# Kernel tuning notes

Hardware: AMD Instinct MI355X
Metric: run time of the kernel (lower is better)

## Reference

```python
import jax, jax.numpy as jnp
import numpy as np

N_QUBITS = 8
N_LAYERS = 4
N_WIRES = N_QUBITS + 1  # circuit uses an extra ancilla wire
B = 16384
D = 512
LN_EPS = 1e-5


def _rx(theta):
    # RX(t) = [[cos(t/2), -i sin(t/2)], [-i sin(t/2), cos(t/2)]]; theta: () or (B,)
    c = jnp.cos(theta / 2).astype(jnp.complex64)
    s = (-1j) * jnp.sin(theta / 2).astype(jnp.complex64)
    return jnp.stack([jnp.stack([c, s], -1), jnp.stack([s, c], -1)], -2)


def _ry(theta):
    c = jnp.cos(theta / 2).astype(jnp.complex64)
    s = jnp.sin(theta / 2).astype(jnp.complex64)
    return jnp.stack([jnp.stack([c, -s], -1), jnp.stack([s, c], -1)], -2)


def _rz(theta):
    # RZ(t) = diag(e^{-it/2}, e^{it/2})
    half = (theta / 2).astype(jnp.complex64)
    em = jnp.exp(-1j * half)
    ep = jnp.exp(1j * half)
    z = jnp.zeros_like(em)
    return jnp.stack([jnp.stack([em, z], -1), jnp.stack([z, ep], -1)], -2)


def _apply_1q(state, U, wire):
    # state: (B,) + (2,)*N_WIRES ; U: (2,2) shared or (B,2,2) per-sample
    ax = 1 + wire
    s = jnp.moveaxis(state, ax, -1)
    if U.ndim == 2:
        s = jnp.einsum('ij,...j->...i', U, s)
    else:
        s = jnp.einsum('bij,b...j->b...i', U, s)
    return jnp.moveaxis(s, -1, ax)


def _cnot(state, c, t):
    # flip target wire t on the control=1 slice of wire c
    s = jnp.moveaxis(state, (1 + c, 1 + t), (-2, -1))
    s = jnp.stack([s[..., 0, :], jnp.flip(s[..., 1, :], axis=-1)], axis=-2)
    return jnp.moveaxis(s, (-2, -1), (1 + c, 1 + t))


def _quantum_circuit(angles, q_weights):
    # angles: (B, N_QUBITS) per-sample data angles; q_weights: (N_LAYERS, N_QUBITS+1)
    b = angles.shape[0]
    state = jnp.zeros((b, 2 ** N_WIRES), jnp.complex64).at[:, 0].set(1.0)
    state = state.reshape((b,) + (2,) * N_WIRES)
    # data encoding: RX, RZ with per-sample angles
    for i in range(N_QUBITS):
        state = _apply_1q(state, _rx(angles[:, i]), i)
        state = _apply_1q(state, _rz(angles[:, i]), i)
    # first variational layer
    for i in range(N_QUBITS):
        state = _apply_1q(state, _rx(q_weights[0, i]), i)
        state = _apply_1q(state, _rz(q_weights[1, i]), i)
    # entangling layers
    for l in range(1, N_LAYERS):
        for i in range(N_QUBITS):
            state = _cnot(state, i, (i + 1) % N_QUBITS)
            state = _apply_1q(state, _ry(q_weights[l, i]), i)
            state = _apply_1q(state, _rz(q_weights[l, i]), i)
        state = _cnot(state, N_QUBITS - 1, N_QUBITS)
        state = _apply_1q(state, _ry(q_weights[l, -1]), N_QUBITS)
    probs = state.real ** 2 + state.imag ** 2
    # <Z_i> = P(q_i=0) - P(q_i=1)
    zs = []
    for i in range(N_QUBITS):
        axes = tuple(1 + j for j in range(N_WIRES) if j != i)
        p = probs.sum(axes)  # (B, 2)
        zs.append(p[:, 0] - p[:, 1])
    return jnp.stack(zs, axis=1)  # (B, N_QUBITS)


def _forward(x, timestep, w_in, b_in, ln_gamma, ln_beta, q_weights, w_out, b_out):
    h = jnp.tanh(x @ w_in.T + b_in)  # (B, 8)
    mu = h.mean(-1, keepdims=True)
    var = ((h - mu) ** 2).mean(-1, keepdims=True)
    h = (h - mu) / jnp.sqrt(var + LN_EPS) * ln_gamma + ln_beta
    angles = h + timestep  # broadcast scalar timestep
    q_out = _quantum_circuit(angles, q_weights)
    out = q_out @ w_out.T + b_out
    return x + out  # input_dim == output_dim -> residual


def setup_inputs() -> dict:
    key = jax.random.key(0)
    ks = jax.random.split(key, 6)
    x = jax.random.normal(ks[0], (B, D), jnp.float32)
    timestep = jax.random.uniform(ks[1], (1,), jnp.float32)
    w_in = jax.random.normal(ks[2], (N_QUBITS, D), jnp.float32) * np.float32(1.0 / np.sqrt(D))
    b_in = jnp.zeros((N_QUBITS,), jnp.float32)
    ln_gamma = jnp.ones((N_QUBITS,), jnp.float32)
    ln_beta = jnp.zeros((N_QUBITS,), jnp.float32)
    q_weights = jax.random.uniform(ks[3], (N_LAYERS, N_QUBITS + 1), jnp.float32, 0.0, 2.0 * np.pi)
    w_out = jax.random.normal(ks[4], (D, N_QUBITS), jnp.float32) * np.float32(1.0 / np.sqrt(N_QUBITS))
    b_out = jnp.zeros((D,), jnp.float32)
    return {'x': x, 'timestep': timestep, 'w_in': w_in, 'b_in': b_in,
            'ln_gamma': ln_gamma, 'ln_beta': ln_beta, 'q_weights': q_weights,
            'w_out': w_out, 'b_out': b_out}


def reference(x, timestep, w_in, b_in, ln_gamma, ln_beta, q_weights, w_out, b_out):
    return _forward(x, timestep, w_in, b_in, ln_gamma, ln_beta, q_weights, w_out, b_out)
```

## Files before the change

kernel.cpp:

```cpp
#include <hip/hip_runtime.h>
#include <math.h>

#define NSAMP 16384
#define ND    512

typedef float f2 __attribute__((ext_vector_type(2)));
__device__ __forceinline__ f2 spl(float x) { return (f2){x, x}; }

template<int CTRL>
__device__ __forceinline__ float dppf(float x) {
  return __int_as_float(__builtin_amdgcn_update_dpp(
      __float_as_int(x), __float_as_int(x), CTRL, 0xF, 0xF, true));
}
template<int CTRL, int RM, int BM>
__device__ __forceinline__ float dppf_keep(float x) {
  return __int_as_float(__builtin_amdgcn_update_dpp(
      __float_as_int(x), __float_as_int(x), CTRL, RM, BM, false));
}
template<int P>
__device__ __forceinline__ float swzf(float x) {
  return __int_as_float(__builtin_amdgcn_ds_swizzle(__float_as_int(x), P));
}
__device__ __forceinline__ float bpermf(int addrB, float x) {
  return __int_as_float(__builtin_amdgcn_ds_bpermute(addrB, __float_as_int(x)));
}

#if __has_builtin(__builtin_amdgcn_permlane16_swap)
#define HAVE_PLSWAP 1
#endif
__device__ __forceinline__ void plswap16(float x, float& a, float& b) {
#ifdef HAVE_PLSWAP
  auto r = __builtin_amdgcn_permlane16_swap(__float_as_uint(x), __float_as_uint(x), false, false);
  a = __uint_as_float(r[0]); b = __uint_as_float(r[1]);
#else
  a = x; b = swzf<0x401F>(x);
#endif
}
__device__ __forceinline__ void plswap32(float x, float& a, float& b) {
#ifdef HAVE_PLSWAP
  auto r = __builtin_amdgcn_permlane32_swap(__float_as_uint(x), __float_as_uint(x), false, false);
  a = __uint_as_float(r[0]); b = __uint_as_float(r[1]);
#else
  a = x; b = __shfl_xor(x, 32, 64);
#endif
}

template<int M>
__device__ __forceinline__ f2 bfly2(f2 x) {
  f2 r;
  if constexpr (M == 1)       { r.x = dppf<0xB1>(x.x);    r.y = dppf<0xB1>(x.y); }
  else if constexpr (M == 2)  { r.x = dppf<0x4E>(x.x);    r.y = dppf<0x4E>(x.y); }
  else if constexpr (M == 8)  { r.x = dppf<0x128>(x.x);   r.y = dppf<0x128>(x.y); }
  else if constexpr (M == 4)  { r.x = swzf<0x101F>(x.x);  r.y = swzf<0x101F>(x.y); }
  else if constexpr (M == 16) { r.x = swzf<0x401F>(x.x);  r.y = swzf<0x401F>(x.y); }
  else                        { r.x = __shfl_xor(x.x, 32, 64); r.y = __shfl_xor(x.y, 32, 64); }
  return r;
}

__device__ __forceinline__ float fold8_allsum(const float* y, int lane) {
  float v4[4];
#pragma unroll
  for (int i = 0; i < 4; ++i) {
    float keep = (lane & 1) ? y[2 * i + 1] : y[2 * i];
    float send = (lane & 1) ? y[2 * i]     : y[2 * i + 1];
    v4[i] = keep + dppf<0xB1>(send);
  }
  float v2[2];
#pragma unroll
  for (int i = 0; i < 2; ++i) {
    float keep = (lane & 2) ? v4[2 * i + 1] : v4[2 * i];
    float send = (lane & 2) ? v4[2 * i]     : v4[2 * i + 1];
    v2[i] = keep + dppf<0x4E>(send);
  }
  float keep = (lane & 4) ? v2[1] : v2[0];
  float send = (lane & 4) ? v2[0] : v2[1];
  float r = keep + swzf<0x101F>(send);
  r += dppf<0x128>(r);
  { float a, b; plswap16(r, a, b); r = a + b; }
  { float a, b; plswap32(r, a, b); r = a + b; }
  return r;
}

__device__ __forceinline__ float grp8_sum(float x) {
  x += dppf<0xB1>(x);
  x += dppf<0x4E>(x);
  x += swzf<0x101F>(x);
  return x;
}

__device__ __forceinline__ f2 cmul(f2 a, f2 b) {
  f2 bs = __builtin_shufflevector(b, b, 1, 0);
  f2 t  = (f2){-a.y, a.y} * bs;
  return spl(a.x) * b + t;
}

template<int LB>
__device__ __forceinline__ void ry_local(f2* s, float c, float sv) {
#pragma unroll
  for (int r0 = 0; r0 < 8; ++r0) {
    if (r0 & (1 << LB)) continue;
    const int r1 = r0 | (1 << LB);
    f2 a0 = s[r0], a1 = s[r1];
    s[r0] = spl(c) * a0 - spl(sv) * a1;
    s[r1] = spl(sv) * a0 + spl(c) * a1;
  }
}
template<int LB>
__device__ __forceinline__ void rz_local(f2* s, f2 phm, f2 php) {
#pragma unroll
  for (int r = 0; r < 8; ++r) s[r] = cmul(s[r], (r & (1 << LB)) ? php : phm);
}
template<int M>
__device__ __forceinline__ void ry_lane(f2* s, float c, float se) {
#pragma unroll
  for (int r = 0; r < 8; ++r) {
    f2 p = bfly2<M>(s[r]);
    s[r] = spl(c) * s[r] + spl(se) * p;
  }
}
template<int CB, int TB>
__device__ __forceinline__ void cnot_ll(f2* s) {
#pragma unroll
  for (int r0 = 0; r0 < 8; ++r0) {
    if (!(r0 & (1 << CB)) || (r0 & (1 << TB))) continue;
    const int r1 = r0 | (1 << TB);
    f2 t = s[r0]; s[r0] = s[r1]; s[r1] = t;
  }
}
template<int CB, int TM>
__device__ __forceinline__ void cnot_lt(f2* s) {
#pragma unroll
  for (int r = 0; r < 8; ++r) {
    if (!(r & (1 << CB))) continue;
    s[r] = bfly2<TM>(s[r]);
  }
}
__device__ __forceinline__ void cnot_bperm(f2* s, int addrB) {
#pragma unroll
  for (int r = 0; r < 8; ++r) {
    s[r].x = bpermf(addrB, s[r].x);
    s[r].y = bpermf(addrB, s[r].y);
  }
}
__device__ __forceinline__ void cnot_m4_t1(f2* s) {
#pragma unroll
  for (int r = 0; r < 8; ++r) {
    s[r].x = dppf_keep<0xB1, 0xF, 0xA>(s[r].x);
    s[r].y = dppf_keep<0xB1, 0xF, 0xA>(s[r].y);
  }
}
__device__ __forceinline__ void cnot_m1_t2(f2* s) {
#pragma unroll
  for (int r = 0; r < 8; ++r) {
    s[r].x = dppf<0x6C>(s[r].x);
    s[r].y = dppf<0x6C>(s[r].y);
  }
}
template<int TB>
__device__ __forceinline__ void cnot_tl(f2* s, bool cc) {
#pragma unroll
  for (int r0 = 0; r0 < 8; ++r0) {
    if (r0 & (1 << TB)) continue;
    const int r1 = r0 | (1 << TB);
    f2 n0, n1;
    n0.x = cc ? s[r1].x : s[r0].x;  n0.y = cc ? s[r1].y : s[r0].y;
    n1.x = cc ? s[r0].x : s[r1].x;  n1.y = cc ? s[r0].y : s[r1].y;
    s[r0] = n0; s[r1] = n1;
  }
}

__global__ void qpre_kernel(const float* __restrict__ qw, float* __restrict__ ws) {
  int t = threadIdx.x;
  if (t < 27) {
    float s, c; __sincosf(qw[9 + t] * 0.5f, &s, &c);
    ws[2 * t] = c; ws[2 * t + 1] = s;
  }
}

template<bool PRE>
struct Consts {
  const float* qw; const float* ws;
  __device__ __forceinline__ f2 ltrig(int l, int i) const {
    if constexpr (PRE) {
      return ((const f2*)ws)[(l - 1) * 9 + i];
    } else {
      float s, c; __sincosf(qw[l * 9 + i] * 0.5f, &s, &c);
      return (f2){c, s};
    }
  }
};

template<bool PRE, int MODE>
__device__ __forceinline__ void do_layer(f2* st, int lane, const Consts<PRE>& cst, int l,
                                         int addr56, int addr67, int addr78) {
  f2 t[9];
#pragma unroll
  for (int i = 0; i < 9; ++i) t[i] = cst.ltrig(l, i);

  cnot_ll<0, 1>(st);
  ry_local<0>(st, t[0].x, t[0].y);
  rz_local<0>(st, (f2){t[0].x, -t[0].y}, (f2){t[0].x, t[0].y});
  cnot_ll<1, 2>(st);
  ry_local<1>(st, t[1].x, t[1].y);
  cnot_lt<2, 4>(st);
  ry_local<2>(st, t[2].x, t[2].y);
  cnot_m4_t1(st);
  { float se = (lane & 4) ? t[3].y : -t[3].y;
    ry_lane<4>(st, t[3].x, se); }
  cnot_m1_t2(st);
  { float se = (lane & 1) ? t[4].y : -t[4].y;
    ry_lane<1>(st, t[4].x, se); }
  cnot_bperm(st, addr56);
  { float se = (lane & 2) ? t[5].y : -t[5].y;
    ry_lane<2>(st, t[5].x, se); }
  cnot_bperm(st, addr67);
  { float se = (lane & 8) ? t[6].y : -t[6].y;
    ry_lane<8>(st, t[6].x, se); }
  cnot_tl<0>(st, (lane & 16) != 0);
  { float se = (lane & 16) ? t[7].y : -t[7].y;
    ry_lane<16>(st, t[7].x, se); }

  if constexpr (MODE == 1) {
    const float wsel = (lane & 32) ? ((lane & 16) ? t[8].x : t[8].y)
                                   : ((lane & 16) ? -t[8].y : t[8].x);
#pragma unroll
    for (int r = 0; r < 8; ++r) st[r] = st[r] * spl(wsel);
  }
  if constexpr (MODE == 2) {
    cnot_bperm(st, addr78);
  }
  if constexpr (MODE != 3) {
    f2 L4[4];
#pragma unroll
    for (int k = 0; k < 4; ++k) {
      f2 p1 = (f2){t[1].x, (k & 1) ? t[1].y : -t[1].y};
      f2 p2 = (f2){t[2].x, (k & 2) ? t[2].y : -t[2].y};
      L4[k] = cmul(p1, p2);
    }
    f2 phW = (f2){t[3].x, (lane & 4)  ? t[3].y : -t[3].y};
    phW = cmul(phW, (f2){t[4].x, (lane & 1)  ? t[4].y : -t[4].y});
    phW = cmul(phW, (f2){t[5].x, (lane & 2)  ? t[5].y : -t[5].y});
    phW = cmul(phW, (f2){t[6].x, (lane & 8)  ? t[6].y : -t[6].y});
    phW = cmul(phW, (f2){t[7].x, (lane & 16) ? t[7].y : -t[7].y});
    f2 pr[4];
#pragma unroll
    for (int k = 0; k < 4; ++k) pr[k] = cmul(L4[k], phW);
#pragma unroll
    for (int r = 0; r < 8; ++r) st[r] = cmul(st[r], pr[(r >> 1) & 3]);
  }
}

template<bool PRE>
__global__ __launch_bounds__(256, 4) void qlayer_kernel(
    const float* __restrict__ x, const float* __restrict__ tstep,
    const float* __restrict__ w_in, const float* __restrict__ b_in,
    const float* __restrict__ g, const float* __restrict__ be,
    const float* __restrict__ qw, const float* __restrict__ w_out,
    const float* __restrict__ b_out, float* __restrict__ out,
    const float* __restrict__ ws)
{
  __shared__ __align__(16) float s_u[4][8][4];
  __shared__ __align__(16) float s_z[4][8];

  const int tid    = threadIdx.x;
  const int lane   = tid & 63;
  const int wv     = tid >> 6;
  const int sample = blockIdx.x * 4 + wv;
  const int jq     = lane & 7;
  const int dbase  = lane << 3;

  const int addr56 = (lane ^ ((lane & 2) << 2)) << 2;
  const int addr67 = (lane ^ ((lane & 8) << 1)) << 2;
  const int addr78 = (lane ^ ((lane & 16) << 1)) << 2;

  const float4* xr4 = (const float4*)(x + (size_t)sample * ND + dbase);
  const float4 xa = xr4[0], xb = xr4[1];
  const f2 xp0 = (f2){xa.x, xa.y}, xp1 = (f2){xa.z, xa.w};
  const f2 xp2 = (f2){xb.x, xb.y}, xp3 = (f2){xb.z, xb.w};

  float h[8];
#pragma unroll
  for (int j = 0; j < 8; ++j) {
    const float4* wj = (const float4*)(w_in + j * ND + dbase);
    float4 wa = wj[0], wb = wj[1];
    f2 acc = xp0 * (f2){wa.x, wa.y};
    acc += xp1 * (f2){wa.z, wa.w};
    acc += xp2 * (f2){wb.x, wb.y};
    acc += xp3 * (f2){wb.z, wb.w};
    h[j] = acc.x + acc.y;
  }
  const float H = fold8_allsum(h, lane);

  const float t0 = tstep[0];
  float tj;
  {
    float v = H + b_in[jq];
    v = fminf(15.f, fmaxf(-15.f, v));
    float e2 = __expf(2.f * v);
    tj = (e2 - 1.f) * __builtin_amdgcn_rcpf(e2 + 1.f);
  }
  const float mu = grp8_sum(tj) * 0.125f;
  const float dv = tj - mu;
  const float var = grp8_sum(dv * dv) * 0.125f;
  const float rstd = rsqrtf(var + 1e-5f);
  const float ang = dv * rstd * g[jq] + be[jq] + t0;

  {
    float sa, ca; __sincosf(ang * 0.5f, &sa, &ca);
    f2 v0 = spl(ca) * (f2){ca, -sa};
    f2 v1 = spl(sa) * (f2){sa, -ca};
    float s0, c0, s1, c1;
    __sincosf(qw[jq] * 0.5f, &s0, &c0);
    __sincosf(qw[9 + jq] * 0.5f, &s1, &c1);
    f2 M00 = (f2){ c1 * c0, -s1 * c0};
    f2 M01 = (f2){-s1 * s0, -c1 * s0};
    f2 M10 = (f2){ s1 * s0, -c1 * s0};
    f2 M11 = (f2){ c1 * c0,  s1 * c0};
    f2 u0 = cmul(M00, v0) + cmul(M01, v1);
    f2 u1 = cmul(M10, v0) + cmul(M11, v1);
    if (lane < 8) {
      float4 uu = {u0.x, u0.y, u1.x, u1.y};
      *(float4*)&s_u[wv][jq][0] = uu;
    }
  }
  asm volatile("s_waitcnt lgkmcnt(0)" ::: "memory");
  __builtin_amdgcn_sched_barrier(0);

  f2 u0a[3], u1a[3];
#pragma unroll
  for (int i = 0; i < 3; ++i) {
    float4 uu = *(const float4*)&s_u[wv][i][0];
    u0a[i] = (f2){uu.x, uu.y};
    u1a[i] = (f2){uu.z, uu.w};
  }
  f2 hl;
  {
    const f2* ub = (const f2*)&s_u[wv][0][0];
    f2 r4 = ub[4 * 2 + ((lane >> 0) & 1)];
    f2 r5 = ub[5 * 2 + ((lane >> 1) & 1)];
    f2 r3 = ub[3 * 2 + ((lane >> 2) & 1)];
    f2 r6 = ub[6 * 2 + ((lane >> 3) & 1)];
    f2 r7 = ub[7 * 2 + ((lane >> 4) & 1)];
    hl = cmul(cmul(cmul(cmul(r4, r5), r3), r6), r7);
  }
  f2 t01[4];
#pragma unroll
  for (int q = 0; q < 4; ++q)
    t01[q] = cmul((q & 1) ? u1a[0] : u0a[0], (q & 2) ? u1a[1] : u0a[1]);
  f2 st[8];
#pragma unroll
  for (int r = 0; r < 8; ++r)
    st[r] = cmul(cmul(t01[r & 3], (r & 4) ? u1a[2] : u0a[2]), hl);

  Consts<PRE> cst{qw, ws};
  do_layer<PRE, 1>(st, lane, cst, 1, addr56, addr67, addr78);
  do_layer<PRE, 2>(st, lane, cst, 2, addr56, addr67, addr78);
  do_layer<PRE, 3>(st, lane, cst, 3, addr56, addr67, addr78);

  float p[8];
#pragma unroll
  for (int r = 0; r < 8; ++r) p[r] = st[r].x * st[r].x + st[r].y * st[r].y;
  float tot = 0.f;
#pragma unroll
  for (int r = 0; r < 8; ++r) tot += p[r];

  float y[8];
  y[0] = (p[0] - p[1]) + (p[2] - p[3]) + (p[4] - p[5]) + (p[6] - p[7]);
  y[1] = (p[0] + p[1]) - (p[2] + p[3]) + (p[4] + p[5]) - (p[6] + p[7]);
  y[2] = (p[0] + p[1] + p[2] + p[3]) - (p[4] + p[5] + p[6] + p[7]);
  y[3] = (lane & 4)  ? -tot : tot;
  y[4] = (lane & 1)  ? -tot : tot;
  y[5] = (lane & 2)  ? -tot : tot;
  y[6] = (lane & 8)  ? -tot : tot;
  y[7] = (lane & 16) ? -tot : tot;
  const float Z = fold8_allsum(y, lane);
  if (lane < 8) s_z[wv][jq] = Z;
  asm volatile("s_waitcnt lgkmcnt(0)" ::: "memory");
  __builtin_amdgcn_sched_barrier(0);

  float4 za = *(const float4*)&s_z[wv][0];
  float4 zb = *(const float4*)&s_z[wv][4];

  const f2 z01 = (f2){za.x, za.y}, z23 = (f2){za.z, za.w};
  const f2 z45 = (f2){zb.x, zb.y}, z67 = (f2){zb.z, zb.w};
  const float4* wo = (const float4*)(w_out + (size_t)dbase * 8);
  const float4* bo = (const float4*)(b_out + dbase);
  const float4 b0 = bo[0], b1 = bo[1];
  const float xk[8] = {xa.x, xa.y, xa.z, xa.w, xb.x, xb.y, xb.z, xb.w};
  const float bk[8] = {b0.x, b0.y, b0.z, b0.w, b1.x, b1.y, b1.z, b1.w};
  float o[8];
#pragma unroll
  for (int k = 0; k < 8; ++k) {
    float4 wa = wo[2 * k];
    float4 wb = wo[2 * k + 1];
    f2 acc = z01 * (f2){wa.x, wa.y};
    acc += z23 * (f2){wa.z, wa.w};
    acc += z45 * (f2){wb.x, wb.y};
    acc += z67 * (f2){wb.z, wb.w};
    o[k] = xk[k] + bk[k] + acc.x + acc.y;
  }
  float4* outp = (float4*)(out + (size_t)sample * ND + dbase);
  outp[0] = (float4){o[0], o[1], o[2], o[3]};
  outp[1] = (float4){o[4], o[5], o[6], o[7]};
}

extern "C" void kernel_launch(void* const* d_in, const int* in_sizes, int n_in,
                              void* d_out, int out_size, void* d_ws, size_t ws_size,
                              hipStream_t stream) {
  const float* x     = (const float*)d_in[0];
  const float* ts    = (const float*)d_in[1];
  const float* w_in  = (const float*)d_in[2];
  const float* b_in  = (const float*)d_in[3];
  const float* g     = (const float*)d_in[4];
  const float* be    = (const float*)d_in[5];
  const float* qw    = (const float*)d_in[6];
  const float* w_out = (const float*)d_in[7];
  const float* b_out = (const float*)d_in[8];
  float* out = (float*)d_out;

  const bool pre = (d_ws != nullptr) && (ws_size >= 256);
  if (pre) {
    qpre_kernel<<<dim3(1), dim3(64), 0, stream>>>(qw, (float*)d_ws);
    qlayer_kernel<true><<<dim3(NSAMP / 4), dim3(256), 0, stream>>>(
        x, ts, w_in, b_in, g, be, qw, w_out, b_out, out, (const float*)d_ws);
  } else {
    qlayer_kernel<false><<<dim3(NSAMP / 4), dim3(256), 0, stream>>>(
        x, ts, w_in, b_in, g, be, qw, w_out, b_out, out, (const float*)d_ws);
  }
}
```

Measured before the change: 58.18 us.

## Map four samples per wavefront with 32 amplitudes per lane

Changes the thread mapping so each 64-lane wavefront handles four samples, with 16 lanes per sample and 32 state amplitudes per lane, instead of one sample per wavefront with 8 amplitudes per lane. More qubits become register-local, so more gates run as in-register swaps and rotations instead of cross-lane DPP, swizzle or bpermute traffic. The cross-32 and cross-16 lane reductions are dropped. Register pressure rises sharply (launch bounds lowered to 3 waves), and each lane now does wider strided loads of x and w_out across 32 columns.

```diff
diff --git a/kernel.cpp b/kernel.cpp
--- a/kernel.cpp
+++ b/kernel.cpp
@@ -12,11 +12,6 @@
   return __int_as_float(__builtin_amdgcn_update_dpp(
       __float_as_int(x), __float_as_int(x), CTRL, 0xF, 0xF, true));
 }
-template<int CTRL, int RM, int BM>
-__device__ __forceinline__ float dppf_keep(float x) {
-  return __int_as_float(__builtin_amdgcn_update_dpp(
-      __float_as_int(x), __float_as_int(x), CTRL, RM, BM, false));
-}
 template<int P>
 __device__ __forceinline__ float swzf(float x) {
   return __int_as_float(__builtin_amdgcn_ds_swizzle(__float_as_int(x), P));
@@ -25,59 +20,34 @@
   return __int_as_float(__builtin_amdgcn_ds_bpermute(addrB, __float_as_int(x)));
 }
 
-#if __has_builtin(__builtin_amdgcn_permlane16_swap)
-#define HAVE_PLSWAP 1
-#endif
-__device__ __forceinline__ void plswap16(float x, float& a, float& b) {
-#ifdef HAVE_PLSWAP
-  auto r = __builtin_amdgcn_permlane16_swap(__float_as_uint(x), __float_as_uint(x), false, false);
-  a = __uint_as_float(r[0]); b = __uint_as_float(r[1]);
-#else
-  a = x; b = swzf<0x401F>(x);
-#endif
-}
-__device__ __forceinline__ void plswap32(float x, float& a, float& b) {
-#ifdef HAVE_PLSWAP
-  auto r = __builtin_amdgcn_permlane32_swap(__float_as_uint(x), __float_as_uint(x), false, false);
-  a = __uint_as_float(r[0]); b = __uint_as_float(r[1]);
-#else
-  a = x; b = __shfl_xor(x, 32, 64);
-#endif
-}
-
 template<int M>
 __device__ __forceinline__ f2 bfly2(f2 x) {
   f2 r;
-  if constexpr (M == 1)       { r.x = dppf<0xB1>(x.x);    r.y = dppf<0xB1>(x.y); }
-  else if constexpr (M == 2)  { r.x = dppf<0x4E>(x.x);    r.y = dppf<0x4E>(x.y); }
-  else if constexpr (M == 8)  { r.x = dppf<0x128>(x.x);   r.y = dppf<0x128>(x.y); }
-  else if constexpr (M == 4)  { r.x = swzf<0x101F>(x.x);  r.y = swzf<0x101F>(x.y); }
-  else if constexpr (M == 16) { r.x = swzf<0x401F>(x.x);  r.y = swzf<0x401F>(x.y); }
-  else                        { r.x = __shfl_xor(x.x, 32, 64); r.y = __shfl_xor(x.y, 32, 64); }
+  if constexpr (M == 1)      { r.x = dppf<0xB1>(x.x);  r.y = dppf<0xB1>(x.y); }
+  else if constexpr (M == 2) { r.x = dppf<0x4E>(x.x);  r.y = dppf<0x4E>(x.y); }
+  else                       { r.x = dppf<0x128>(x.x); r.y = dppf<0x128>(x.y); }
   return r;
 }
 
-__device__ __forceinline__ float fold8_allsum(const float* y, int lane) {
+__device__ __forceinline__ float fold16_allsum(const float* y, int gl) {
   float v4[4];
 #pragma unroll
   for (int i = 0; i < 4; ++i) {
-    float keep = (lane & 1) ? y[2 * i + 1] : y[2 * i];
-    float send = (lane & 1) ? y[2 * i]     : y[2 * i + 1];
+    float keep = (gl & 1) ? y[2 * i + 1] : y[2 * i];
+    float send = (gl & 1) ? y[2 * i]     : y[2 * i + 1];
     v4[i] = keep + dppf<0xB1>(send);
   }
   float v2[2];
 #pragma unroll
   for (int i = 0; i < 2; ++i) {
-    float keep = (lane & 2) ? v4[2 * i + 1] : v4[2 * i];
-    float send = (lane & 2) ? v4[2 * i]     : v4[2 * i + 1];
+    float keep = (gl & 2) ? v4[2 * i + 1] : v4[2 * i];
+    float send = (gl & 2) ? v4[2 * i]     : v4[2 * i + 1];
     v2[i] = keep + dppf<0x4E>(send);
   }
-  float keep = (lane & 4) ? v2[1] : v2[0];
-  float send = (lane & 4) ? v2[0] : v2[1];
+  float keep = (gl & 4) ? v2[1] : v2[0];
+  float send = (gl & 4) ? v2[0] : v2[1];
   float r = keep + swzf<0x101F>(send);
   r += dppf<0x128>(r);
-  { float a, b; plswap16(r, a, b); r = a + b; }
-  { float a, b; plswap32(r, a, b); r = a + b; }
   return r;
 }
 
@@ -97,7 +67,7 @@
 template<int LB>
 __device__ __forceinline__ void ry_local(f2* s, float c, float sv) {
 #pragma unroll
-  for (int r0 = 0; r0 < 8; ++r0) {
+  for (int r0 = 0; r0 < 32; ++r0) {
     if (r0 & (1 << LB)) continue;
     const int r1 = r0 | (1 << LB);
     f2 a0 = s[r0], a1 = s[r1];
@@ -108,12 +78,12 @@
 template<int LB>
 __device__ __forceinline__ void rz_local(f2* s, f2 phm, f2 php) {
 #pragma unroll
-  for (int r = 0; r < 8; ++r) s[r] = cmul(s[r], (r & (1 << LB)) ? php : phm);
+  for (int r = 0; r < 32; ++r) s[r] = cmul(s[r], (r & (1 << LB)) ? php : phm);
 }
 template<int M>
 __device__ __forceinline__ void ry_lane(f2* s, float c, float se) {
 #pragma unroll
-  for (int r = 0; r < 8; ++r) {
+  for (int r = 0; r < 32; ++r) {
     f2 p = bfly2<M>(s[r]);
     s[r] = spl(c) * s[r] + spl(se) * p;
   }
@@ -121,7 +91,7 @@
 template<int CB, int TB>
 __device__ __forceinline__ void cnot_ll(f2* s) {
 #pragma unroll
-  for (int r0 = 0; r0 < 8; ++r0) {
+  for (int r0 = 0; r0 < 32; ++r0) {
     if (!(r0 & (1 << CB)) || (r0 & (1 << TB))) continue;
     const int r1 = r0 | (1 << TB);
     f2 t = s[r0]; s[r0] = s[r1]; s[r1] = t;
@@ -130,28 +100,21 @@
 template<int CB, int TM>
 __device__ __forceinline__ void cnot_lt(f2* s) {
 #pragma unroll
-  for (int r = 0; r < 8; ++r) {
+  for (int r = 0; r < 32; ++r) {
     if (!(r & (1 << CB))) continue;
     s[r] = bfly2<TM>(s[r]);
   }
 }
 __device__ __forceinline__ void cnot_bperm(f2* s, int addrB) {
 #pragma unroll
-  for (int r = 0; r < 8; ++r) {
+  for (int r = 0; r < 32; ++r) {
     s[r].x = bpermf(addrB, s[r].x);
     s[r].y = bpermf(addrB, s[r].y);
   }
 }
-__device__ __forceinline__ void cnot_m4_t1(f2* s) {
-#pragma unroll
-  for (int r = 0; r < 8; ++r) {
-    s[r].x = dppf_keep<0xB1, 0xF, 0xA>(s[r].x);
-    s[r].y = dppf_keep<0xB1, 0xF, 0xA>(s[r].y);
-  }
-}
 __device__ __forceinline__ void cnot_m1_t2(f2* s) {
 #pragma unroll
-  for (int r = 0; r < 8; ++r) {
+  for (int r = 0; r < 32; ++r) {
     s[r].x = dppf<0x6C>(s[r].x);
     s[r].y = dppf<0x6C>(s[r].y);
   }
@@ -159,7 +122,7 @@
 template<int TB>
 __device__ __forceinline__ void cnot_tl(f2* s, bool cc) {
 #pragma unroll
-  for (int r0 = 0; r0 < 8; ++r0) {
+  for (int r0 = 0; r0 < 32; ++r0) {
     if (r0 & (1 << TB)) continue;
     const int r1 = r0 | (1 << TB);
     f2 n0, n1;
@@ -192,7 +155,7 @@
 
 template<bool PRE, int MODE>
 __device__ __forceinline__ void do_layer(f2* st, int lane, const Consts<PRE>& cst, int l,
-                                         int addr56, int addr67, int addr78) {
+                                         int addr67, int addr78) {
   f2 t[9];
 #pragma unroll
   for (int i = 0; i < 9; ++i) t[i] = cst.ltrig(l, i);
@@ -202,56 +165,50 @@
   rz_local<0>(st, (f2){t[0].x, -t[0].y}, (f2){t[0].x, t[0].y});
   cnot_ll<1, 2>(st);
   ry_local<1>(st, t[1].x, t[1].y);
-  cnot_lt<2, 4>(st);
+  cnot_ll<2, 3>(st);
   ry_local<2>(st, t[2].x, t[2].y);
-  cnot_m4_t1(st);
-  { float se = (lane & 4) ? t[3].y : -t[3].y;
-    ry_lane<4>(st, t[3].x, se); }
+  cnot_ll<3, 4>(st);
+  ry_local<3>(st, t[3].x, t[3].y);
+  cnot_lt<4, 1>(st);
+  ry_local<4>(st, t[4].x, t[4].y);
   cnot_m1_t2(st);
-  { float se = (lane & 1) ? t[4].y : -t[4].y;
-    ry_lane<1>(st, t[4].x, se); }
-  cnot_bperm(st, addr56);
-  { float se = (lane & 2) ? t[5].y : -t[5].y;
-    ry_lane<2>(st, t[5].x, se); }
+  { float se = (lane & 1) ? t[5].y : -t[5].y;
+    ry_lane<1>(st, t[5].x, se); }
   cnot_bperm(st, addr67);
-  { float se = (lane & 8) ? t[6].y : -t[6].y;
-    ry_lane<8>(st, t[6].x, se); }
-  cnot_tl<0>(st, (lane & 16) != 0);
-  { float se = (lane & 16) ? t[7].y : -t[7].y;
-    ry_lane<16>(st, t[7].x, se); }
-
-  if constexpr (MODE == 1) {
-    const float wsel = (lane & 32) ? ((lane & 16) ? t[8].x : t[8].y)
-                                   : ((lane & 16) ? -t[8].y : t[8].x);
-#pragma unroll
-    for (int r = 0; r < 8; ++r) st[r] = st[r] * spl(wsel);
-  }
+  { float se = (lane & 2) ? t[6].y : -t[6].y;
+    ry_lane<2>(st, t[6].x, se); }
+  cnot_tl<0>(st, (lane & 8) != 0);
+  { float se = (lane & 8) ? t[7].y : -t[7].y;
+    ry_lane<8>(st, t[7].x, se); }
+
   if constexpr (MODE == 2) {
     cnot_bperm(st, addr78);
   }
   if constexpr (MODE != 3) {
-    f2 L4[4];
-#pragma unroll
-    for (int k = 0; k < 4; ++k) {
-      f2 p1 = (f2){t[1].x, (k & 1) ? t[1].y : -t[1].y};
-      f2 p2 = (f2){t[2].x, (k & 2) ? t[2].y : -t[2].y};
-      L4[k] = cmul(p1, p2);
-    }
-    f2 phW = (f2){t[3].x, (lane & 4)  ? t[3].y : -t[3].y};
-    phW = cmul(phW, (f2){t[4].x, (lane & 1)  ? t[4].y : -t[4].y});
-    phW = cmul(phW, (f2){t[5].x, (lane & 2)  ? t[5].y : -t[5].y});
-    phW = cmul(phW, (f2){t[6].x, (lane & 8)  ? t[6].y : -t[6].y});
-    phW = cmul(phW, (f2){t[7].x, (lane & 16) ? t[7].y : -t[7].y});
-    f2 pr[4];
-#pragma unroll
-    for (int k = 0; k < 4; ++k) pr[k] = cmul(L4[k], phW);
-#pragma unroll
-    for (int r = 0; r < 8; ++r) st[r] = cmul(st[r], pr[(r >> 1) & 3]);
+    f2 phW = (f2){t[5].x, (lane & 1) ? t[5].y : -t[5].y};
+    phW = cmul(phW, (f2){t[6].x, (lane & 2) ? t[6].y : -t[6].y});
+    phW = cmul(phW, (f2){t[7].x, (lane & 8) ? t[7].y : -t[7].y});
+    if constexpr (MODE == 1) {
+      const float wsel = (lane & 4) ? ((lane & 8) ? t[8].x : t[8].y)
+                                    : ((lane & 8) ? -t[8].y : t[8].x);
+      phW = phW * spl(wsel);
+    }
+    f2 P1[2], P2[4], P3[8], P4[16];
+    P1[0] = cmul(phW, (f2){t[1].x, -t[1].y});
+    P1[1] = cmul(phW, (f2){t[1].x,  t[1].y});
+#pragma unroll
+    for (int k = 0; k < 4; ++k)  P2[k] = cmul(P1[k & 1], (f2){t[2].x, (k & 2) ? t[2].y : -t[2].y});
+#pragma unroll
+    for (int k = 0; k < 8; ++k)  P3[k] = cmul(P2[k & 3], (f2){t[3].x, (k & 4) ? t[3].y : -t[3].y});
+#pragma unroll
+    for (int k = 0; k < 16; ++k) P4[k] = cmul(P3[k & 7], (f2){t[4].x, (k & 8) ? t[4].y : -t[4].y});
+#pragma unroll
+    for (int r = 0; r < 32; ++r) st[r] = cmul(st[r], P4[(r >> 1) & 15]);
   }
 }
 
 template<bool PRE>
-__global__ __launch_bounds__(256, 4) void qlayer_kernel(
+__global__ __launch_bounds__(256, 3) void qlayer_kernel(
     const float* __restrict__ x, const float* __restrict__ tstep,
     const float* __restrict__ w_in, const float* __restrict__ b_in,
     const float* __restrict__ g, const float* __restrict__ be,
@@ -259,37 +216,41 @@
     const float* __restrict__ b_out, float* __restrict__ out,
     const float* __restrict__ ws)
 {
-  __shared__ __align__(16) float s_u[4][8][4];
-  __shared__ __align__(16) float s_z[4][8];
+  __shared__ __align__(16) float s_u[4][4][8][4];
+  __shared__ __align__(16) float s_z[4][4][8];
 
   const int tid    = threadIdx.x;
   const int lane   = tid & 63;
   const int wv     = tid >> 6;
-  const int sample = blockIdx.x * 4 + wv;
-  const int jq     = lane & 7;
-  const int dbase  = lane << 3;
-
-  const int addr56 = (lane ^ ((lane & 2) << 2)) << 2;
-  const int addr67 = (lane ^ ((lane & 8) << 1)) << 2;
-  const int addr78 = (lane ^ ((lane & 16) << 1)) << 2;
+  const int gl     = lane & 15;
+  const int smp    = lane >> 4;
+  const int sample = blockIdx.x * 16 + wv * 4 + smp;
+  const int jq     = gl & 7;
+  const int dbase  = gl << 5;
+
+  const int addr67 = (lane ^ ((lane & 2) << 2)) << 2;
+  const int addr78 = (lane ^ ((lane & 8) >> 1)) << 2;
 
   const float4* xr4 = (const float4*)(x + (size_t)sample * ND + dbase);
-  const float4 xa = xr4[0], xb = xr4[1];
-  const f2 xp0 = (f2){xa.x, xa.y}, xp1 = (f2){xa.z, xa.w};
-  const f2 xp2 = (f2){xb.x, xb.y}, xp3 = (f2){xb.z, xb.w};
-
   float h[8];
-#pragma unroll
-  for (int j = 0; j < 8; ++j) {
-    const float4* wj = (const float4*)(w_in + j * ND + dbase);
-    float4 wa = wj[0], wb = wj[1];
-    f2 acc = xp0 * (f2){wa.x, wa.y};
-    acc += xp1 * (f2){wa.z, wa.w};
-    acc += xp2 * (f2){wb.x, wb.y};
-    acc += xp3 * (f2){wb.z, wb.w};
-    h[j] = acc.x + acc.y;
-  }
-  const float H = fold8_allsum(h, lane);
+  {
+    float4 xv[8];
+#pragma unroll
+    for (int m = 0; m < 8; ++m) xv[m] = xr4[m];
+#pragma unroll
+    for (int j = 0; j < 8; ++j) {
+      const float4* wj = (const float4*)(w_in + j * ND + dbase);
+      f2 acc = (f2){0.f, 0.f};
+#pragma unroll
+      for (int m = 0; m < 8; ++m) {
+        float4 w = wj[m];
+        acc += (f2){xv[m].x, xv[m].y} * (f2){w.x, w.y};
+        acc += (f2){xv[m].z, xv[m].w} * (f2){w.z, w.w};
+      }
+      h[j] = acc.x + acc.y;
+    }
+  }
+  const float H = fold16_allsum(h, gl);
 
   const float t0 = tstep[0];
   float tj;
@@ -299,16 +260,12 @@
     float e2 = __expf(2.f * v);
     tj = (e2 - 1.f) * __builtin_amdgcn_rcpf(e2 + 1.f);
   }
-  const float mu = grp8_sum(tj) * 0.125f;
-  const float dv = tj - mu;
+  const float mu  = grp8_sum(tj) * 0.125f;
+  const float dv  = tj - mu;
   const float var = grp8_sum(dv * dv) * 0.125f;
-  const float rstd = rsqrtf(var + 1e-5f);
-  const float ang = dv * rstd * g[jq] + be[jq] + t0;
+  const float ang = dv * rsqrtf(var + 1e-5f) * g[jq] + be[jq] + t0;
 
   {
-    float sa, ca; __sincosf(ang * 0.5f, &sa, &ca);
-    f2 v0 = spl(ca) * (f2){ca, -sa};
-    f2 v1 = spl(sa) * (f2){sa, -ca};
     float s0, c0, s1, c1;
     __sincosf(qw[jq] * 0.5f, &s0, &c0);
     __sincosf(qw[9 + jq] * 0.5f, &s1, &c1);
@@ -316,92 +273,103 @@
     f2 M01 = (f2){-s1 * s0, -c1 * s0};
     f2 M10 = (f2){ s1 * s0, -c1 * s0};
     f2 M11 = (f2){ c1 * c0,  s1 * c0};
+    float sa, ca; __sincosf(ang * 0.5f, &sa, &ca);
+    f2 v0 = spl(ca) * (f2){ca, -sa};
+    f2 v1 = spl(sa) * (f2){sa, -ca};
     f2 u0 = cmul(M00, v0) + cmul(M01, v1);
     f2 u1 = cmul(M10, v0) + cmul(M11, v1);
-    if (lane < 8) {
-      float4 uu = {u0.x, u0.y, u1.x, u1.y};
-      *(float4*)&s_u[wv][jq][0] = uu;
+    if (gl < 8) {
+      *(float4*)&s_u[wv][smp][jq][0] = (float4){u0.x, u0.y, u1.x, u1.y};
     }
   }
   asm volatile("s_waitcnt lgkmcnt(0)" ::: "memory");
   __builtin_amdgcn_sched_barrier(0);
 
-  f2 u0a[3], u1a[3];
-#pragma unroll
-  for (int i = 0; i < 3; ++i) {
-    float4 uu = *(const float4*)&s_u[wv][i][0];
-    u0a[i] = (f2){uu.x, uu.y};
-    u1a[i] = (f2){uu.z, uu.w};
-  }
-  f2 hl;
+  f2 st[32];
   {
-    const f2* ub = (const f2*)&s_u[wv][0][0];
-    f2 r4 = ub[4 * 2 + ((lane >> 0) & 1)];
-    f2 r5 = ub[5 * 2 + ((lane >> 1) & 1)];
-    f2 r3 = ub[3 * 2 + ((lane >> 2) & 1)];
-    f2 r6 = ub[6 * 2 + ((lane >> 3) & 1)];
-    f2 r7 = ub[7 * 2 + ((lane >> 4) & 1)];
-    hl = cmul(cmul(cmul(cmul(r4, r5), r3), r6), r7);
-  }
-  f2 t01[4];
-#pragma unroll
-  for (int q = 0; q < 4; ++q)
-    t01[q] = cmul((q & 1) ? u1a[0] : u0a[0], (q & 2) ? u1a[1] : u0a[1]);
-  f2 st[8];
-#pragma unroll
-  for (int r = 0; r < 8; ++r)
-    st[r] = cmul(cmul(t01[r & 3], (r & 4) ? u1a[2] : u0a[2]), hl);
+    const f2* ub = (const f2*)&s_u[wv][smp][0][0];
+    f2 r5 = ub[5 * 2 + ((lane >> 0) & 1)];
+    f2 r6 = ub[6 * 2 + ((lane >> 1) & 1)];
+    f2 r7 = ub[7 * 2 + ((lane >> 3) & 1)];
+    f2 hl = cmul(cmul(r5, r6), r7);
+    f2 w1[2];
+#pragma unroll
+    for (int b = 0; b < 2; ++b) w1[b] = cmul(ub[0 * 2 + b], hl);
+    f2 w2[4];
+#pragma unroll
+    for (int r = 0; r < 4; ++r) w2[r] = cmul(w1[r & 1], ub[1 * 2 + ((r >> 1) & 1)]);
+    f2 w3[8];
+#pragma unroll
+    for (int r = 0; r < 8; ++r) w3[r] = cmul(w2[r & 3], ub[2 * 2 + ((r >> 2) & 1)]);
+    f2 w4[16];
+#pragma unroll
+    for (int r = 0; r < 16; ++r) w4[r] = cmul(w3[r & 7], ub[3 * 2 + ((r >> 3) & 1)]);
+#pragma unroll
+    for (int r = 0; r < 32; ++r) st[r] = cmul(w4[r & 15], ub[4 * 2 + ((r >> 4) & 1)]);
+  }
 
   Consts<PRE> cst{qw, ws};
-  do_layer<PRE, 1>(st, lane, cst, 1, addr56, addr67, addr78);
-  do_layer<PRE, 2>(st, lane, cst, 2, addr56, addr67, addr78);
-  do_layer<PRE, 3>(st, lane, cst, 3, addr56, addr67, addr78);
-
-  float p[8];
-#pragma unroll
-  for (int r = 0; r < 8; ++r) p[r] = st[r].x * st[r].x + st[r].y * st[r].y;
-  float tot = 0.f;
-#pragma unroll
-  for (int r = 0; r < 8; ++r) tot += p[r];
+  do_layer<PRE, 1>(st, lane, cst, 1, addr67, addr78);
+  do_layer<PRE, 2>(st, lane, cst, 2, addr67, addr78);
+  do_layer<PRE, 3>(st, lane, cst, 3, addr67, addr78);
+
+  float p[32];
+#pragma unroll
+  for (int r = 0; r < 32; ++r) p[r] = st[r].x * st[r].x + st[r].y * st[r].y;
 
   float y[8];
-  y[0] = (p[0] - p[1]) + (p[2] - p[3]) + (p[4] - p[5]) + (p[6] - p[7]);
-  y[1] = (p[0] + p[1]) - (p[2] + p[3]) + (p[4] + p[5]) - (p[6] + p[7]);
-  y[2] = (p[0] + p[1] + p[2] + p[3]) - (p[4] + p[5] + p[6] + p[7]);
-  y[3] = (lane & 4)  ? -tot : tot;
-  y[4] = (lane & 1)  ? -tot : tot;
-  y[5] = (lane & 2)  ? -tot : tot;
-  y[6] = (lane & 8)  ? -tot : tot;
-  y[7] = (lane & 16) ? -tot : tot;
-  const float Z = fold8_allsum(y, lane);
-  if (lane < 8) s_z[wv][jq] = Z;
+  float q1[16]; { float d = 0.f;
+#pragma unroll
+    for (int k = 0; k < 16; ++k) { q1[k] = p[2*k] + p[2*k+1]; d += p[2*k] - p[2*k+1]; }
+    y[0] = d; }
+  float q2[8]; { float d = 0.f;
+#pragma unroll
+    for (int k = 0; k < 8; ++k) { q2[k] = q1[2*k] + q1[2*k+1]; d += q1[2*k] - q1[2*k+1]; }
+    y[1] = d; }
+  float q3[4]; { float d = 0.f;
+#pragma unroll
+    for (int k = 0; k < 4; ++k) { q3[k] = q2[2*k] + q2[2*k+1]; d += q2[2*k] - q2[2*k+1]; }
+    y[2] = d; }
+  float q4[2];
+  q4[0] = q3[0] + q3[1]; q4[1] = q3[2] + q3[3];
+  y[3] = (q3[0] - q3[1]) + (q3[2] - q3[3]);
+  y[4] = q4[0] - q4[1];
+  const float tot = q4[0] + q4[1];
+  y[5] = (lane & 1) ? -tot : tot;
+  y[6] = (lane & 2) ? -tot : tot;
+  y[7] = (lane & 8) ? -tot : tot;
+
+  const float Z = fold16_allsum(y, gl);
+  if (gl < 8) s_z[wv][smp][jq] = Z;
   asm volatile("s_waitcnt lgkmcnt(0)" ::: "memory");
   __builtin_amdgcn_sched_barrier(0);
 
-  float4 za = *(const float4*)&s_z[wv][0];
-  float4 zb = *(const float4*)&s_z[wv][4];
+  const float4 za = *(const float4*)&s_z[wv][smp][0];
+  const float4 zb = *(const float4*)&s_z[wv][smp][4];
 
   const f2 z01 = (f2){za.x, za.y}, z23 = (f2){za.z, za.w};
   const f2 z45 = (f2){zb.x, zb.y}, z67 = (f2){zb.z, zb.w};
-  const float4* wo = (const float4*)(w_out + (size_t)dbase * 8);
-  const float4* bo = (const float4*)(b_out + dbase);
-  const float4 b0 = bo[0], b1 = bo[1];
-  const float xk[8] = {xa.x, xa.y, xa.z, xa.w, xb.x, xb.y, xb.z, xb.w};
-  const float bk[8] = {b0.x, b0.y, b0.z, b0.w, b1.x, b1.y, b1.z, b1.w};
-  float o[8];
+  const float4* wo4 = (const float4*)w_out;
+  const float4* bo4 = (const float4*)(b_out + dbase);
+  float* outrow = out + (size_t)sample * ND + dbase;
 #pragma unroll
   for (int k = 0; k < 8; ++k) {
-    float4 wa = wo[2 * k];
-    float4 wb = wo[2 * k + 1];
-    f2 acc = z01 * (f2){wa.x, wa.y};
-    acc += z23 * (f2){wa.z, wa.w};
-    acc += z45 * (f2){wb.x, wb.y};
-    acc += z67 * (f2){wb.z, wb.w};
-    o[k] = xk[k] + bk[k] + acc.x + acc.y;
-  }
-  float4* outp = (float4*)(out + (size_t)sample * ND + dbase);
-  outp[0] = (float4){o[0], o[1], o[2], o[3]};
-  outp[1] = (float4){o[4], o[5], o[6], o[7]};
+    float4 xk = xr4[k];
+    float4 bk = bo4[k];
+    float o[4];
+#pragma unroll
+    for (int e = 0; e < 4; ++e) {
+      int d = dbase + k * 4 + e;
+      float4 wa = wo4[2 * d];
+      float4 wb = wo4[2 * d + 1];
+      f2 acc = z01 * (f2){wa.x, wa.y};
+      acc += z23 * (f2){wa.z, wa.w};
+      acc += z45 * (f2){wb.x, wb.y};
+      acc += z67 * (f2){wb.z, wb.w};
+      o[e] = ((const float*)&xk)[e] + ((const float*)&bk)[e] + acc.x + acc.y;
+    }
+    ((float4*)outrow)[k] = (float4){o[0], o[1], o[2], o[3]};
+  }
 }
 
 extern "C" void kernel_launch(void* const* d_in, const int* in_sizes, int n_in,
@@ -421,10 +389,10 @@
   const bool pre = (d_ws != nullptr) && (ws_size >= 256);
   if (pre) {
     qpre_kernel<<<dim3(1), dim3(64), 0, stream>>>(qw, (float*)d_ws);
-    qlayer_kernel<true><<<dim3(NSAMP / 4), dim3(256), 0, stream>>>(
+    qlayer_kernel<true><<<dim3(NSAMP / 16), dim3(256), 0, stream>>>(
         x, ts, w_in, b_in, g, be, qw, w_out, b_out, out, (const float*)d_ws);
   } else {
-    qlayer_kernel<false><<<dim3(NSAMP / 4), dim3(256), 0, stream>>>(
+    qlayer_kernel<false><<<dim3(NSAMP / 16), dim3(256), 0, stream>>>(
         x, ts, w_in, b_in, g, be, qw, w_out, b_out, out, (const float*)d_ws);
   }
 }
```

Result: slower. 101.8 us (+75.0%).
